# Kernel optimization log

Measured on AMD Instinct MI355X. Metric: run time of the kernel, lower is better.

Reference implementation:

```python
import jax, jax.numpy as jnp
import numpy as np

B, QT, N, E, H = 4, 1024, 2048, 512, 8
Dh = E // H
ROPE_BASE = 10000.0


def rope_cos_sin_from_pos(pos_idx, Dh, base=10000.0, dtype=jnp.float32):
    # pos_idx: [B, T] -> cos, sin: [B, T, Dh]
    half = Dh // 2
    freqs = 1.0 / base ** (jnp.arange(0, half, dtype=dtype) / half)
    ang = pos_idx.astype(dtype)[..., None] * freqs[None, None, :]
    cos = jnp.repeat(jnp.cos(ang), 2, axis=-1)
    sin = jnp.repeat(jnp.sin(ang), 2, axis=-1)
    return cos, sin


def rope_apply(x_hd, cos, sin):
    # x_hd: [B, H, T, Dh]; cos/sin: [B, 1, T, Dh] (only first Dh//2 used, as in source)
    D = x_hd.shape[-1]
    x2 = x_hd.reshape(*x_hd.shape[:-1], D // 2, 2)
    x1, xi = x2[..., 0], x2[..., 1]
    c = cos[..., :D // 2]
    s = sin[..., :D // 2]
    y1 = x1 * c - xi * s
    y2 = x1 * s + xi * c
    return jnp.stack([y1, y2], axis=-1).reshape(*x_hd.shape)


def setup_inputs() -> dict:
    key = jax.random.key(0)
    ks = jax.random.split(key, 16)
    scale_w = 1.0 / np.sqrt(E)
    inp = {
        "q": jax.random.normal(ks[0], (B, QT, E), jnp.float32),
        "kv": jax.random.normal(ks[1], (B, N, E), jnp.float32),
        "q_mask": jax.random.randint(ks[2], (B, QT), 0, 2) > 0,
        "kv_mask": jax.random.randint(ks[3], (B, N), 0, 2) > 0,
        "q_pos_idx": jnp.sort(jax.random.randint(ks[4], (B, QT), 0, 4096), axis=-1).astype(jnp.int32),
        "kv_pos_idx": jnp.sort(jax.random.randint(ks[5], (B, N), 0, 4096), axis=-1).astype(jnp.int32),
        "Wq": jax.random.normal(ks[6], (E, E), jnp.float32) * scale_w,
        "bq": jnp.zeros((E,), jnp.float32),
        "Wk": jax.random.normal(ks[7], (E, E), jnp.float32) * scale_w,
        "bk": jnp.zeros((E,), jnp.float32),
        "Wv": jax.random.normal(ks[8], (E, E), jnp.float32) * scale_w,
        "bv": jnp.zeros((E,), jnp.float32),
        "Wo": jax.random.normal(ks[9], (E, E), jnp.float32) * scale_w,
        "bo": jnp.zeros((E,), jnp.float32),
    }
    return inp


def reference(q, kv, q_mask, kv_mask, q_pos_idx, kv_pos_idx,
              Wq, bq, Wk, bk, Wv, bv, Wo, bo):
    scale = 1.0 / jnp.sqrt(jnp.array(Dh, dtype=q.dtype))
    # projections -> [B, H, T, Dh]
    qh = (q @ Wq + bq).reshape(B, QT, H, Dh).transpose(0, 2, 1, 3)
    kh = (kv @ Wk + bk).reshape(B, N, H, Dh).transpose(0, 2, 1, 3)
    vh = (kv @ Wv + bv).reshape(B, N, H, Dh).transpose(0, 2, 1, 3)
    # per-sample RoPE
    cos_q, sin_q = rope_cos_sin_from_pos(q_pos_idx, Dh, ROPE_BASE, qh.dtype)
    cos_k, sin_k = rope_cos_sin_from_pos(kv_pos_idx, Dh, ROPE_BASE, kh.dtype)
    qh = rope_apply(qh, cos_q[:, None], sin_q[:, None])
    kh = rope_apply(kh, cos_k[:, None], sin_k[:, None])
    # scores [B, H, Q, N]
    scores = jnp.einsum("bhqd,bhkd->bhqk", qh, kh) * scale
    kvm = kv_mask[:, None, None, :].astype(bool)
    scores = jnp.where(kvm, scores, jnp.full_like(scores, -1e9))
    attn = jax.nn.softmax(scores, axis=-1)
    # dropout_rate=0 / deterministic -> identity; post-softmax mask + renorm
    attn = attn * kvm
    attn = attn / (attn.sum(-1, keepdims=True) + 1e-9)
    ctx = jnp.einsum("bhqk,bhkd->bhqd", attn, vh)
    ctx = ctx.transpose(0, 2, 1, 3).reshape(B, QT, E)
    ctx = ctx @ Wo + bo
    ctx = ctx * q_mask.astype(ctx.dtype)[:, :, None]
    return ctx, attn
```

## Files before the change

kernel.cpp:

```cpp
#include <hip/hip_runtime.h>
#include <hip/hip_bf16.h>

#define B_  4
#define QT_ 1024
#define N_  2048
#define E_  512
#define H_  8
#define DH_ 64

typedef float  f32x4  __attribute__((ext_vector_type(4)));
typedef __bf16 bf16x8 __attribute__((ext_vector_type(8)));
typedef unsigned short u16;
typedef u16 u16x4 __attribute__((ext_vector_type(4)));

static __device__ __forceinline__ u16 f2bf(float f) {
    unsigned u = __builtin_bit_cast(unsigned, f);
    return (u16)((u + 0x7fffu + ((u >> 16) & 1u)) >> 16);
}

static __device__ __forceinline__ bf16x8 ldbf8(const u16* p) {
    uint4 v = *reinterpret_cast<const uint4*>(p);
    return __builtin_bit_cast(bf16x8, v);
}

#define MFMA16(a, b, c) __builtin_amdgcn_mfma_f32_16x16x32_bf16((a), (b), (c), 0, 0, 0)

static __device__ __forceinline__ void g2lds16(const u16* g, u16* l) {
    __builtin_amdgcn_global_load_lds((__attribute__((address_space(1))) void*)(void*)g,
                                     (__attribute__((address_space(3))) void*)l, 16, 0, 0);
}

__global__ __launch_bounds__(256) void cvt_all(const float* __restrict__ q,
                                               const float* __restrict__ kv,
                                               u16* __restrict__ qbf,
                                               u16* __restrict__ kvbf) {
    const int QN4 = B_ * QT_ * E_ / 4;
    int i = blockIdx.x * 256 + threadIdx.x;
    const float4* s;
    ushort4* d;
    if (i < QN4) {
        s = reinterpret_cast<const float4*>(q) + i;
        d = reinterpret_cast<ushort4*>(qbf) + i;
    } else {
        int j = i - QN4;
        s = reinterpret_cast<const float4*>(kv) + j;
        d = reinterpret_cast<ushort4*>(kvbf) + j;
    }
    float4 v = *s;
    ushort4 o;
    o.x = f2bf(v.x); o.y = f2bf(v.y); o.z = f2bf(v.z); o.w = f2bf(v.w);
    *d = o;
}

__global__ __launch_bounds__(256) void wt_all(const float* __restrict__ Wq,
                                              const float* __restrict__ Wk,
                                              const float* __restrict__ Wv,
                                              const float* __restrict__ Wo,
                                              u16* __restrict__ wt4) {
    __shared__ float t[64][65];
    const float* W = (blockIdx.z == 0) ? Wq : (blockIdx.z == 1) ? Wk : (blockIdx.z == 2) ? Wv : Wo;
    u16* dst = wt4 + (size_t)blockIdx.z * E_ * E_;
    int k0 = blockIdx.x * 64, n0 = blockIdx.y * 64;
    int tid = threadIdx.x;
#pragma unroll
    for (int i = 0; i < 16; i++) {
        int idx = tid + i * 256, r = idx >> 6, c = idx & 63;
        t[r][c] = W[(k0 + r) * E_ + n0 + c];
    }
    __syncthreads();
#pragma unroll
    for (int i = 0; i < 16; i++) {
        int idx = tid + i * 256, r = idx >> 6, c = idx & 63;
        dst[(n0 + r) * E_ + k0 + c] = f2bf(t[c][r]);
    }
}

__global__ __launch_bounds__(256) void rope_all(const int* __restrict__ qpos,
                                                const int* __restrict__ kvpos,
                                                float2* __restrict__ tq,
                                                float2* __restrict__ tk) {
    const int QROWS = B_ * QT_;
    int i = blockIdx.x * 256 + threadIdx.x;
    int k = i & 15, row = i >> 4;
    float fr = exp2f((float)k * -0.41524101186092028f);
    int p;
    float2* dst;
    if (row < QROWS) { p = qpos[row]; dst = tq + i; }
    else { p = kvpos[row - QROWS]; dst = tk + (i - QROWS * 16); }
    float sn, cs;
    sincosf((float)p * fr, &sn, &cs);
    *dst = make_float2(cs, sn);
}

__global__ __launch_bounds__(256) void proj_qkv(const u16* __restrict__ qbf,
                                                const u16* __restrict__ kvbf,
                                                const u16* __restrict__ wt4,
                                                const float* __restrict__ bq,
                                                const float* __restrict__ bk,
                                                const float* __restrict__ bv,
                                                u16* __restrict__ qhh,
                                                u16* __restrict__ khh,
                                                u16* __restrict__ vt,
                                                const float2* __restrict__ tq,
                                                const float2* __restrict__ tk) {
    __shared__ __align__(16) u16 la[2][128 * 32];
    __shared__ __align__(16) u16 lb[2][128 * 32];

    const int id = blockIdx.x;
    const int sw = (id & 7) * 80 + (id >> 3);
    const bool isQ = (sw < 128);
    int m0, n0;
    const u16 *X, *W;
    if (isQ) { m0 = (sw >> 2) * 128; n0 = (sw & 3) * 128; X = qbf; W = wt4; }
    else { const int s2 = sw - 128; m0 = (s2 >> 3) * 128; n0 = (s2 & 7) * 128; X = kvbf; W = wt4 + 512 * 512; }

    const int tid = threadIdx.x, w = tid >> 6, lane = tid & 63;
    const int lr = lane & 15, lg = lane >> 4;
    const int wml = (w >> 1) * 64, wnl = (w & 1) * 64;

    auto stage = [&](const u16* gsrc, u16* lbuf) {
#pragma unroll
        for (int i = 0; i < 2; i++) {
            const int r0 = w * 32 + i * 16;
            const int row = r0 + (lane >> 2);
            const u16* src = gsrc + row * E_ + (((lane & 3) ^ (row & 3)) * 8);
            g2lds16(src, lbuf + r0 * 32);
        }
    };

    f32x4 acc[4][4];
#pragma unroll
    for (int i = 0; i < 4; i++)
#pragma unroll
        for (int j = 0; j < 4; j++) acc[i][j] = f32x4{0.f, 0.f, 0.f, 0.f};

    stage(X + m0 * E_, la[0]);
    stage(W + n0 * E_, lb[0]);
    __syncthreads();
    int buf = 0;
    for (int kt = 0; kt < E_ / 32; kt++) {
        if (kt + 1 < E_ / 32) {
            stage(X + m0 * E_ + (kt + 1) * 32, la[buf ^ 1]);
            stage(W + n0 * E_ + (kt + 1) * 32, lb[buf ^ 1]);
        }
        bf16x8 a[4], bb[4];
#pragma unroll
        for (int mb = 0; mb < 4; mb++) {
            const int r = wml + mb * 16 + lr;
            a[mb] = ldbf8(la[buf] + r * 32 + ((lg ^ (r & 3)) * 8));
        }
#pragma unroll
        for (int nb = 0; nb < 4; nb++) {
            const int r = wnl + nb * 16 + lr;
            bb[nb] = ldbf8(lb[buf] + r * 32 + ((lg ^ (r & 3)) * 8));
        }
        __builtin_amdgcn_s_setprio(1);
#pragma unroll
        for (int mb = 0; mb < 4; mb++)
#pragma unroll
            for (int nb = 0; nb < 4; nb++)
                acc[mb][nb] = MFMA16(a[mb], bb[nb], acc[mb][nb]);
        __builtin_amdgcn_s_setprio(0);
        __syncthreads();
        buf ^= 1;
    }

    const bool isV = !isQ && (n0 >= 512);
#pragma unroll
    for (int mb = 0; mb < 4; mb++) {
#pragma unroll
        for (int nb = 0; nb < 4; nb++) {
            const int col = n0 + wnl + nb * 16 + lr;
            const float bs = isQ ? bq[col] : (isV ? bv[col - 512] : bk[col]);
#pragma unroll
            for (int r = 0; r < 4; r++) {
                const int row = m0 + wml + mb * 16 + lg * 4 + r;
                float v = acc[mb][nb][r] + bs;
                if (isV) {
                    const int cv = col - 512, d = cv & 63, h = cv >> 6;
                    const int b = row >> 11, n = row & 2047;
                    vt[(((b * H_ + h) * (N_ / 64) + (n >> 6)) * DH_ + d) * 64 + (n & 63)] = f2bf(v);
                } else {
                    const int d = col & 63, h = col >> 6;
                    float2 t = isQ ? tq[row * 16 + (d >> 2)] : tk[row * 16 + (d >> 2)];
                    float other = __shfl_xor(v, 1);
                    float y = (d & 1) ? (other * t.y + v * t.x) : (v * t.x - other * t.y);
                    if (isQ) {
                        y *= 0.125f;
                        const int b = row >> 10, tok = row & 1023;
                        qhh[((b * H_ + h) * QT_ + tok) * DH_ + d] = f2bf(y);
                    } else {
                        const int b = row >> 11, tok = row & 2047;
                        khh[((b * H_ + h) * N_ + tok) * DH_ + d] = f2bf(y);
                    }
                }
            }
        }
    }
}

__global__ __launch_bounds__(256) void attn_sums(const u16* __restrict__ qh,
                                                 const u16* __restrict__ kh,
                                                 const int* __restrict__ kv_mask,
                                                 float* __restrict__ sums4) {
    __shared__ __align__(16) u16 kbuf[2][64 * 64];

    const int id = blockIdx.x;
    const int sw = (id & 7) * 256 + (id >> 3);
    const int bh = sw >> 6, qt = (sw >> 2) & 15, ns = sw & 3;
    const int b = bh >> 3;
    const int tid = threadIdx.x, w = tid >> 6, lane = tid & 63;
    const int lr = lane & 15, lg = lane >> 4;
    const int q0 = qt * 64 + w * 16;

    const u16* qbase = qh + (bh * QT_ + q0) * DH_;
    const bf16x8 qf0 = ldbf8(qbase + lr * DH_ + lg * 8);
    const bf16x8 qf1 = ldbf8(qbase + lr * DH_ + 32 + lg * 8);
    const u16* kbase = kh + (size_t)bh * (N_ * DH_) + ns * 512 * DH_;
    const int* mbase = kv_mask + b * N_ + ns * 512;

    auto stage = [&](const u16* gsrc, u16* lbuf) {
#pragma unroll
        for (int i = 0; i < 2; i++) {
            const int r0 = w * 16 + i * 8;
            const int row = r0 + (lane >> 3);
            const u16* src = gsrc + row * 64 + (((lane & 7) ^ (row & 7)) * 8);
            g2lds16(src, lbuf + r0 * 64);
        }
    };

    float lsum[4] = {0.f, 0.f, 0.f, 0.f};
    stage(kbase, kbuf[0]);
    __syncthreads();
    for (int t = 0; t < 8; t++) {
        const u16* kc = kbuf[t & 1];
        if (t < 7) stage(kbase + (t + 1) * (64 * DH_), kbuf[(t + 1) & 1]);
#pragma unroll
        for (int n = 0; n < 4; n++) {
            const int krow = n * 16 + lr;
            const u16* kp = kc + krow * 64;
            bf16x8 k0 = ldbf8(kp + ((lg ^ (krow & 7)) * 8));
            bf16x8 k1 = ldbf8(kp + (((lg + 4) ^ (krow & 7)) * 8));
            f32x4 c = f32x4{0.f, 0.f, 0.f, 0.f};
            __builtin_amdgcn_s_setprio(1);
            c = MFMA16(qf0, k0, c);
            c = MFMA16(qf1, k1, c);
            __builtin_amdgcn_s_setprio(0);
            const bool keep = (mbase[t * 64 + n * 16 + lr] != 0);
#pragma unroll
            for (int r = 0; r < 4; r++) lsum[r] += keep ? __expf(c[r]) : 0.f;
        }
        __syncthreads();
    }
#pragma unroll
    for (int r = 0; r < 4; r++) {
        float s = lsum[r];
        s += __shfl_xor(s, 1); s += __shfl_xor(s, 2);
        s += __shfl_xor(s, 4); s += __shfl_xor(s, 8);
        if (lr == 0) sums4[((size_t)bh * QT_ + q0 + lg * 4 + r) * 4 + ns] = s;
    }
}

__global__ __launch_bounds__(512) void attn_pv(const u16* __restrict__ qh,
                                               const u16* __restrict__ kh,
                                               const u16* __restrict__ vt,
                                               const int* __restrict__ kv_mask,
                                               const float* __restrict__ sums4,
                                               float* __restrict__ attn_out,
                                               float* __restrict__ pvpart) {
    __shared__ __align__(16) u16 kbuf[2][64 * 64];
    __shared__ __align__(16) u16 vbuf[2][64 * 64];
    __shared__ unsigned PW[8][16][32];

    const int id = blockIdx.x;
    const int sw = (id & 7) * 128 + (id >> 3);
    const int bh = sw >> 5, qt = (sw >> 2) & 7, ns = sw & 3;
    const int b = bh >> 3;
    const int tid = threadIdx.x, w = tid >> 6, lane = tid & 63;
    const int lr = lane & 15, lg = lane >> 4;
    const int q0 = qt * 128 + w * 16;

    const u16* qbase = qh + (bh * QT_ + q0) * DH_;
    const bf16x8 qf0 = ldbf8(qbase + lr * DH_ + lg * 8);
    const bf16x8 qf1 = ldbf8(qbase + lr * DH_ + 32 + lg * 8);
    const u16* kbase = kh + (size_t)bh * (N_ * DH_) + ns * 512 * DH_;
    const u16* vbase = vt + (size_t)bh * (N_ * DH_) + ns * 512 * DH_;
    const int* mbase = kv_mask + b * N_ + ns * 512;

    float inv[4];
#pragma unroll
    for (int r = 0; r < 4; r++) {
        float4 s4 = *reinterpret_cast<const float4*>(
            sums4 + ((size_t)bh * QT_ + q0 + lg * 4 + r) * 4);
        float tot = s4.x + s4.y + s4.z + s4.w;
        inv[r] = (tot > 0.f) ? (1.0f / tot) : 0.f;
    }

    auto stage = [&](int t, u16* kb, u16* vb) {
        const int r0 = w * 8;
        const int row = r0 + (lane >> 3);
        const int gsw = ((lane & 7) ^ (row & 7)) * 8;
        g2lds16(kbase + (t * 64 + row) * 64 + gsw, kb + r0 * 64);
        g2lds16(vbase + (t * 64 + row) * 64 + gsw, vb + r0 * 64);
    };

    f32x4 pv[4];
#pragma unroll
    for (int i = 0; i < 4; i++) pv[i] = f32x4{0.f, 0.f, 0.f, 0.f};
    unsigned(*P)[32] = PW[w];
    float* abase = attn_out + ((size_t)(bh * QT_ + q0)) * N_ + ns * 512;
    const int srow = lane >> 4, cq = lane & 15;

    stage(0, kbuf[0], vbuf[0]);
    __syncthreads();
    for (int t = 0; t < 8; t++) {
        const u16* kc = kbuf[t & 1];
        const u16* vc = vbuf[t & 1];
        if (t < 7) stage(t + 1, kbuf[(t + 1) & 1], vbuf[(t + 1) & 1]);
#pragma unroll
        for (int n = 0; n < 4; n++) {
            const int krow = n * 16 + lr;
            const u16* kp = kc + krow * 64;
            bf16x8 k0 = ldbf8(kp + ((lg ^ (krow & 7)) * 8));
            bf16x8 k1 = ldbf8(kp + (((lg + 4) ^ (krow & 7)) * 8));
            f32x4 c = f32x4{0.f, 0.f, 0.f, 0.f};
            __builtin_amdgcn_s_setprio(1);
            c = MFMA16(qf0, k0, c);
            c = MFMA16(qf1, k1, c);
            __builtin_amdgcn_s_setprio(0);
            const bool keep = (mbase[t * 64 + n * 16 + lr] != 0);
#pragma unroll
            for (int r = 0; r < 4; r++) {
                float p = keep ? (__expf(c[r]) * inv[r]) : 0.f;
                float hi = __shfl_xor(p, 1);
                __bf16 lo_b = (__bf16)p, hi_b = (__bf16)hi;
                unsigned pk = ((unsigned)__builtin_bit_cast(u16, hi_b) << 16) |
                              (unsigned)__builtin_bit_cast(u16, lo_b);
                if (!(lr & 1)) {
                    const int row = lg * 4 + r, c32 = n * 8 + (lr >> 1);
                    P[row][(((c32 >> 2) ^ (row & 7)) << 2) + (c32 & 3)] = pk;
                }
            }
        }
#pragma unroll
        for (int i = 0; i < 4; i++) {
            const int row = i * 4 + srow, rw = row & 7;
            const int m = (((cq >> 1) ^ rw) << 2) + ((cq & 1) << 1);
            uint2 pp = *reinterpret_cast<const uint2*>(&P[row][m]);
            f32x4 vv;
            vv[0] = __builtin_bit_cast(float, pp.x << 16);
            vv[1] = __builtin_bit_cast(float, pp.x & 0xffff0000u);
            vv[2] = __builtin_bit_cast(float, pp.y << 16);
            vv[3] = __builtin_bit_cast(float, pp.y & 0xffff0000u);
            *reinterpret_cast<f32x4*>(abase + (size_t)row * N_ + t * 64 + cq * 4) = vv;
        }
#pragma unroll
        for (int ks = 0; ks < 2; ks++) {
            const int g = (4 * ks + lg) ^ (lr & 7);
            uint4 a4 = *reinterpret_cast<const uint4*>(&P[lr][g << 2]);
            bf16x8 af = __builtin_bit_cast(bf16x8, a4);
            __builtin_amdgcn_s_setprio(1);
#pragma unroll
            for (int nb = 0; nb < 4; nb++) {
                const int vrow = nb * 16 + lr;
                bf16x8 bv = ldbf8(vc + vrow * 64 + (((ks * 4 + lg) ^ (vrow & 7)) * 8));
                pv[nb] = MFMA16(af, bv, pv[nb]);
            }
            __builtin_amdgcn_s_setprio(0);
        }
        __syncthreads();
    }

    float* pbase = pvpart + (((size_t)ns * 32 + bh) * QT_) * DH_;
#pragma unroll
    for (int nb = 0; nb < 4; nb++)
#pragma unroll
        for (int r = 0; r < 4; r++)
            pbase[(size_t)(q0 + lg * 4 + r) * DH_ + nb * 16 + lr] = pv[nb][r];
}

__global__ __launch_bounds__(256) void ctx_reduce(const float* __restrict__ pvpart,
                                                  u16* __restrict__ ctx) {
    const size_t SL = (size_t)32 * QT_ * DH_;
    const int i = blockIdx.x * 256 + threadIdx.x;
    const int base = i * 4;
    const int d = base & 63, h = (base >> 6) & 7;
    const int bt = base >> 9;
    const size_t pi = (((size_t)(bt >> 10) * 8 + h) * QT_ + (bt & 1023)) * DH_ + d;
    f32x4 s0 = *reinterpret_cast<const f32x4*>(pvpart + pi);
    f32x4 s1 = *reinterpret_cast<const f32x4*>(pvpart + SL + pi);
    f32x4 s2 = *reinterpret_cast<const f32x4*>(pvpart + 2 * SL + pi);
    f32x4 s3 = *reinterpret_cast<const f32x4*>(pvpart + 3 * SL + pi);
    u16x4 o;
#pragma unroll
    for (int j = 0; j < 4; j++) o[j] = f2bf((s0[j] + s1[j]) + (s2[j] + s3[j]));
    *reinterpret_cast<u16x4*>(ctx + base) = o;
}

__global__ __launch_bounds__(256) void proj_o(const u16* __restrict__ X,
                                              const u16* __restrict__ Wt,
                                              const float* __restrict__ bias,
                                              float* __restrict__ outp,
                                              const int* __restrict__ qmask) {
    __shared__ __align__(16) u16 la[2][64 * 64];
    __shared__ __align__(16) u16 lb[2][64 * 64];

    const int id = blockIdx.x;
    const int sw = (id & 7) * 64 + (id >> 3);
    const int m0 = (sw >> 3) * 64, n0 = (sw & 7) * 64;

    const int tid = threadIdx.x, w = tid >> 6, lane = tid & 63;
    const int lr = lane & 15, lg = lane >> 4;
    const int wml = (w >> 1) * 32, wnl = (w & 1) * 32;

    auto stage = [&](const u16* gsrc, u16* lbuf) {
#pragma unroll
        for (int i = 0; i < 2; i++) {
            const int r0 = w * 16 + i * 8;
            const int row = r0 + (lane >> 3);
            const u16* src = gsrc + row * E_ + (((lane & 7) ^ (row & 7)) * 8);
            g2lds16(src, lbuf + r0 * 64);
        }
    };

    f32x4 acc[2][2];
#pragma unroll
    for (int i = 0; i < 2; i++)
#pragma unroll
        for (int j = 0; j < 2; j++) acc[i][j] = f32x4{0.f, 0.f, 0.f, 0.f};

    stage(X + m0 * E_, la[0]);
    stage(Wt + n0 * E_, lb[0]);
    __syncthreads();
    int buf = 0;
    for (int kt = 0; kt < E_ / 64; kt++) {
        if (kt + 1 < E_ / 64) {
            stage(X + m0 * E_ + (kt + 1) * 64, la[buf ^ 1]);
            stage(Wt + n0 * E_ + (kt + 1) * 64, lb[buf ^ 1]);
        }
#pragma unroll
        for (int ks = 0; ks < 2; ks++) {
            bf16x8 a[2], bb[2];
#pragma unroll
            for (int mb = 0; mb < 2; mb++) {
                const int r = wml + mb * 16 + lr;
                a[mb] = ldbf8(la[buf] + r * 64 + (((ks * 4 + lg) ^ (r & 7)) * 8));
            }
#pragma unroll
            for (int nb = 0; nb < 2; nb++) {
                const int r = wnl + nb * 16 + lr;
                bb[nb] = ldbf8(lb[buf] + r * 64 + (((ks * 4 + lg) ^ (r & 7)) * 8));
            }
            __builtin_amdgcn_s_setprio(1);
#pragma unroll
            for (int mb = 0; mb < 2; mb++)
#pragma unroll
                for (int nb = 0; nb < 2; nb++)
                    acc[mb][nb] = MFMA16(a[mb], bb[nb], acc[mb][nb]);
            __builtin_amdgcn_s_setprio(0);
        }
        __syncthreads();
        buf ^= 1;
    }

#pragma unroll
    for (int mb = 0; mb < 2; mb++) {
#pragma unroll
        for (int nb = 0; nb < 2; nb++) {
            const int col = n0 + wnl + nb * 16 + lr;
            const float bs = bias[col];
#pragma unroll
            for (int r = 0; r < 4; r++) {
                const int row = m0 + wml + mb * 16 + lg * 4 + r;
                float v = acc[mb][nb][r] + bs;
                float m = (qmask[row] != 0) ? 1.0f : 0.0f;
                outp[row * E_ + col] = v * m;
            }
        }
    }
}

extern "C" void kernel_launch(void* const* d_in, const int* in_sizes, int n_in,
                              void* d_out, int out_size, void* d_ws, size_t ws_size,
                              hipStream_t stream) {
    (void)in_sizes; (void)n_in; (void)out_size; (void)ws_size;
    const float* q   = (const float*)d_in[0];
    const float* kv  = (const float*)d_in[1];
    const int* q_mask  = (const int*)d_in[2];
    const int* kv_mask = (const int*)d_in[3];
    const int* q_pos   = (const int*)d_in[4];
    const int* kv_pos  = (const int*)d_in[5];
    const float* Wq = (const float*)d_in[6];  const float* bq = (const float*)d_in[7];
    const float* Wk = (const float*)d_in[8];  const float* bk = (const float*)d_in[9];
    const float* Wv = (const float*)d_in[10]; const float* bv = (const float*)d_in[11];
    const float* Wo = (const float*)d_in[12]; const float* bo = (const float*)d_in[13];
    float* outp = (float*)d_out;

    char* ws = (char*)d_ws;
    size_t off = 0;
    auto carve = [&](size_t bytes) -> void* {
        void* p = ws + off;
        off = (off + bytes + 255) & ~(size_t)255;
        return p;
    };
    u16* qbf    = (u16*)carve((size_t)B_ * QT_ * E_ * 2);
    u16* kvbf   = (u16*)carve((size_t)B_ * N_ * E_ * 2);
    u16* wt4    = (u16*)carve((size_t)4 * E_ * E_ * 2);
    u16* qhh    = (u16*)carve((size_t)B_ * H_ * QT_ * DH_ * 2);
    u16* khh    = (u16*)carve((size_t)B_ * H_ * N_ * DH_ * 2);
    u16* vt     = (u16*)carve((size_t)B_ * H_ * DH_ * N_ * 2);
    u16* ctx    = (u16*)carve((size_t)B_ * QT_ * E_ * 2);
    float2* tq  = (float2*)carve((size_t)B_ * QT_ * 16 * sizeof(float2));
    float2* tk  = (float2*)carve((size_t)B_ * N_ * 16 * sizeof(float2));
    float* sums4  = (float*)carve((size_t)B_ * H_ * QT_ * 4 * sizeof(float));
    float* pvpart = (float*)carve((size_t)4 * B_ * H_ * QT_ * DH_ * sizeof(float));

    cvt_all<<<6144, 256, 0, stream>>>(q, kv, qbf, kvbf);
    wt_all<<<dim3(8, 8, 4), 256, 0, stream>>>(Wq, Wk, Wv, Wo, wt4);
    rope_all<<<768, 256, 0, stream>>>(q_pos, kv_pos, tq, tk);

    proj_qkv<<<640, 256, 0, stream>>>(qbf, kvbf, wt4, bq, bk, bv, qhh, khh, vt, tq, tk);

    attn_sums<<<2048, 256, 0, stream>>>(qhh, khh, kv_mask, sums4);
    attn_pv<<<1024, 512, 0, stream>>>(qhh, khh, vt, kv_mask, sums4,
                                      outp + (size_t)B_ * QT_ * E_, pvpart);
    ctx_reduce<<<2048, 256, 0, stream>>>(pvpart, ctx);

    proj_o<<<512, 256, 0, stream>>>(ctx, wt4 + 3 * 512 * 512, bo, outp, q_mask);
}
```

Before: 159.0 us.

## Double query rows per warp in attn_pv and fuse prep kernels

Each warp in attn_pv now handles 32 query rows instead of 16. Every K and V fragment read from LDS feeds two MFMAs, halving K/V staging traffic per query, and the grid shrinks to 512 blocks. The three preprocessing kernels (convert to bf16, weight transpose, RoPE table) are merged into one launch to cut launch overhead. The trade-off is higher register pressure, a larger P scratch buffer in LDS, and fewer blocks to fill the GPU.

```diff
diff --git a/kernel.cpp b/kernel.cpp
--- a/kernel.cpp
+++ b/kernel.cpp
@@ -30,66 +30,68 @@
                                      (__attribute__((address_space(3))) void*)l, 16, 0, 0);
 }
 
-__global__ __launch_bounds__(256) void cvt_all(const float* __restrict__ q,
-                                               const float* __restrict__ kv,
-                                               u16* __restrict__ qbf,
-                                               u16* __restrict__ kvbf) {
-    const int QN4 = B_ * QT_ * E_ / 4;
-    int i = blockIdx.x * 256 + threadIdx.x;
-    const float4* s;
-    ushort4* d;
-    if (i < QN4) {
-        s = reinterpret_cast<const float4*>(q) + i;
-        d = reinterpret_cast<ushort4*>(qbf) + i;
-    } else {
-        int j = i - QN4;
-        s = reinterpret_cast<const float4*>(kv) + j;
-        d = reinterpret_cast<ushort4*>(kvbf) + j;
-    }
-    float4 v = *s;
-    ushort4 o;
-    o.x = f2bf(v.x); o.y = f2bf(v.y); o.z = f2bf(v.z); o.w = f2bf(v.w);
-    *d = o;
-}
-
-__global__ __launch_bounds__(256) void wt_all(const float* __restrict__ Wq,
-                                              const float* __restrict__ Wk,
-                                              const float* __restrict__ Wv,
-                                              const float* __restrict__ Wo,
-                                              u16* __restrict__ wt4) {
-    __shared__ float t[64][65];
-    const float* W = (blockIdx.z == 0) ? Wq : (blockIdx.z == 1) ? Wk : (blockIdx.z == 2) ? Wv : Wo;
-    u16* dst = wt4 + (size_t)blockIdx.z * E_ * E_;
-    int k0 = blockIdx.x * 64, n0 = blockIdx.y * 64;
-    int tid = threadIdx.x;
-#pragma unroll
-    for (int i = 0; i < 16; i++) {
-        int idx = tid + i * 256, r = idx >> 6, c = idx & 63;
-        t[r][c] = W[(k0 + r) * E_ + n0 + c];
-    }
-    __syncthreads();
-#pragma unroll
-    for (int i = 0; i < 16; i++) {
-        int idx = tid + i * 256, r = idx >> 6, c = idx & 63;
-        dst[(n0 + r) * E_ + k0 + c] = f2bf(t[c][r]);
-    }
-}
-
-__global__ __launch_bounds__(256) void rope_all(const int* __restrict__ qpos,
+__global__ __launch_bounds__(256) void prep_all(const float* __restrict__ q,
+                                                const float* __restrict__ kv,
+                                                const float* __restrict__ Wq,
+                                                const float* __restrict__ Wk,
+                                                const float* __restrict__ Wv,
+                                                const float* __restrict__ Wo,
+                                                const int* __restrict__ qpos,
                                                 const int* __restrict__ kvpos,
+                                                u16* __restrict__ qbf,
+                                                u16* __restrict__ kvbf,
+                                                u16* __restrict__ wt4,
                                                 float2* __restrict__ tq,
                                                 float2* __restrict__ tk) {
-    const int QROWS = B_ * QT_;
-    int i = blockIdx.x * 256 + threadIdx.x;
-    int k = i & 15, row = i >> 4;
-    float fr = exp2f((float)k * -0.41524101186092028f);
-    int p;
-    float2* dst;
-    if (row < QROWS) { p = qpos[row]; dst = tq + i; }
-    else { p = kvpos[row - QROWS]; dst = tk + (i - QROWS * 16); }
-    float sn, cs;
-    sincosf((float)p * fr, &sn, &cs);
-    *dst = make_float2(cs, sn);
+    __shared__ float t[64][65];
+    const int bid = blockIdx.x, tid = threadIdx.x;
+    if (bid < 6144) {
+        const int QN4 = B_ * QT_ * E_ / 4;
+        int i = bid * 256 + tid;
+        const float4* s;
+        ushort4* d;
+        if (i < QN4) {
+            s = reinterpret_cast<const float4*>(q) + i;
+            d = reinterpret_cast<ushort4*>(qbf) + i;
+        } else {
+            int j = i - QN4;
+            s = reinterpret_cast<const float4*>(kv) + j;
+            d = reinterpret_cast<ushort4*>(kvbf) + j;
+        }
+        float4 v = *s;
+        ushort4 o;
+        o.x = f2bf(v.x); o.y = f2bf(v.y); o.z = f2bf(v.z); o.w = f2bf(v.w);
+        *d = o;
+    } else if (bid < 6400) {
+        const int idx = bid - 6144;
+        const int z = idx >> 6, rem = idx & 63, xb = rem & 7, yb = rem >> 3;
+        const float* W = (z == 0) ? Wq : (z == 1) ? Wk : (z == 2) ? Wv : Wo;
+        u16* dst = wt4 + (size_t)z * E_ * E_;
+        const int k0 = xb * 64, n0 = yb * 64;
+#pragma unroll
+        for (int i = 0; i < 16; i++) {
+            int ix = tid + i * 256, r = ix >> 6, c = ix & 63;
+            t[r][c] = W[(k0 + r) * E_ + n0 + c];
+        }
+        __syncthreads();
+#pragma unroll
+        for (int i = 0; i < 16; i++) {
+            int ix = tid + i * 256, r = ix >> 6, c = ix & 63;
+            dst[(n0 + r) * E_ + k0 + c] = f2bf(t[c][r]);
+        }
+    } else {
+        const int QROWS = B_ * QT_;
+        int i = (bid - 6400) * 256 + tid;
+        int k = i & 15, row = i >> 4;
+        float fr = exp2f((float)k * -0.41524101186092028f);
+        int p;
+        float2* dst;
+        if (row < QROWS) { p = qpos[row]; dst = tq + i; }
+        else { p = kvpos[row - QROWS]; dst = tk + (i - QROWS * 16); }
+        float sn, cs;
+        sincosf((float)p * fr, &sn, &cs);
+        *dst = make_float2(cs, sn);
+    }
 }
 
 __global__ __launch_bounds__(256) void proj_qkv(const u16* __restrict__ qbf,
@@ -261,40 +263,46 @@
     }
 }
 
-__global__ __launch_bounds__(512) void attn_pv(const u16* __restrict__ qh,
-                                               const u16* __restrict__ kh,
-                                               const u16* __restrict__ vt,
-                                               const int* __restrict__ kv_mask,
-                                               const float* __restrict__ sums4,
-                                               float* __restrict__ attn_out,
-                                               float* __restrict__ pvpart) {
+__global__ __launch_bounds__(512, 4) void attn_pv(const u16* __restrict__ qh,
+                                                  const u16* __restrict__ kh,
+                                                  const u16* __restrict__ vt,
+                                                  const int* __restrict__ kv_mask,
+                                                  const float* __restrict__ sums4,
+                                                  float* __restrict__ attn_out,
+                                                  float* __restrict__ pvpart) {
     __shared__ __align__(16) u16 kbuf[2][64 * 64];
     __shared__ __align__(16) u16 vbuf[2][64 * 64];
-    __shared__ unsigned PW[8][16][32];
+    __shared__ unsigned PW[8][32][32];
 
     const int id = blockIdx.x;
-    const int sw = (id & 7) * 128 + (id >> 3);
-    const int bh = sw >> 5, qt = (sw >> 2) & 7, ns = sw & 3;
+    const int sw = (id & 7) * 64 + (id >> 3);
+    const int bh = sw >> 4, qt = (sw >> 2) & 3, ns = sw & 3;
     const int b = bh >> 3;
     const int tid = threadIdx.x, w = tid >> 6, lane = tid & 63;
     const int lr = lane & 15, lg = lane >> 4;
-    const int q0 = qt * 128 + w * 16;
+    const int q0 = qt * 256 + w * 32;
 
     const u16* qbase = qh + (bh * QT_ + q0) * DH_;
-    const bf16x8 qf0 = ldbf8(qbase + lr * DH_ + lg * 8);
-    const bf16x8 qf1 = ldbf8(qbase + lr * DH_ + 32 + lg * 8);
+    bf16x8 qf[2][2];
+#pragma unroll
+    for (int mq = 0; mq < 2; mq++) {
+        qf[mq][0] = ldbf8(qbase + (mq * 16 + lr) * DH_ + lg * 8);
+        qf[mq][1] = ldbf8(qbase + (mq * 16 + lr) * DH_ + 32 + lg * 8);
+    }
     const u16* kbase = kh + (size_t)bh * (N_ * DH_) + ns * 512 * DH_;
     const u16* vbase = vt + (size_t)bh * (N_ * DH_) + ns * 512 * DH_;
     const int* mbase = kv_mask + b * N_ + ns * 512;
 
-    float inv[4];
-#pragma unroll
-    for (int r = 0; r < 4; r++) {
-        float4 s4 = *reinterpret_cast<const float4*>(
-            sums4 + ((size_t)bh * QT_ + q0 + lg * 4 + r) * 4);
-        float tot = s4.x + s4.y + s4.z + s4.w;
-        inv[r] = (tot > 0.f) ? (1.0f / tot) : 0.f;
-    }
+    float inv[2][4];
+#pragma unroll
+    for (int mq = 0; mq < 2; mq++)
+#pragma unroll
+        for (int r = 0; r < 4; r++) {
+            float4 s4 = *reinterpret_cast<const float4*>(
+                sums4 + ((size_t)bh * QT_ + q0 + mq * 16 + lg * 4 + r) * 4);
+            float tot = s4.x + s4.y + s4.z + s4.w;
+            inv[mq][r] = (tot > 0.f) ? (1.0f / tot) : 0.f;
+        }
 
     auto stage = [&](int t, u16* kb, u16* vb) {
         const int r0 = w * 8;
@@ -304,9 +312,11 @@
         g2lds16(vbase + (t * 64 + row) * 64 + gsw, vb + r0 * 64);
     };
 
-    f32x4 pv[4];
-#pragma unroll
-    for (int i = 0; i < 4; i++) pv[i] = f32x4{0.f, 0.f, 0.f, 0.f};
+    f32x4 pv[2][4];
+#pragma unroll
+    for (int mq = 0; mq < 2; mq++)
+#pragma unroll
+        for (int i = 0; i < 4; i++) pv[mq][i] = f32x4{0.f, 0.f, 0.f, 0.f};
     unsigned(*P)[32] = PW[w];
     float* abase = attn_out + ((size_t)(bh * QT_ + q0)) * N_ + ns * 512;
     const int srow = lane >> 4, cq = lane & 15;
@@ -323,27 +333,33 @@
             const u16* kp = kc + krow * 64;
             bf16x8 k0 = ldbf8(kp + ((lg ^ (krow & 7)) * 8));
             bf16x8 k1 = ldbf8(kp + (((lg + 4) ^ (krow & 7)) * 8));
-            f32x4 c = f32x4{0.f, 0.f, 0.f, 0.f};
+            f32x4 c0 = f32x4{0.f, 0.f, 0.f, 0.f};
+            f32x4 c1 = f32x4{0.f, 0.f, 0.f, 0.f};
             __builtin_amdgcn_s_setprio(1);
-            c = MFMA16(qf0, k0, c);
-            c = MFMA16(qf1, k1, c);
+            c0 = MFMA16(qf[0][0], k0, c0);
+            c0 = MFMA16(qf[0][1], k1, c0);
+            c1 = MFMA16(qf[1][0], k0, c1);
+            c1 = MFMA16(qf[1][1], k1, c1);
             __builtin_amdgcn_s_setprio(0);
-            const bool keep = (mbase[t * 64 + n * 16 + lr] != 0);
-#pragma unroll
-            for (int r = 0; r < 4; r++) {
-                float p = keep ? (__expf(c[r]) * inv[r]) : 0.f;
-                float hi = __shfl_xor(p, 1);
-                __bf16 lo_b = (__bf16)p, hi_b = (__bf16)hi;
-                unsigned pk = ((unsigned)__builtin_bit_cast(u16, hi_b) << 16) |
-                              (unsigned)__builtin_bit_cast(u16, lo_b);
-                if (!(lr & 1)) {
-                    const int row = lg * 4 + r, c32 = n * 8 + (lr >> 1);
-                    P[row][(((c32 >> 2) ^ (row & 7)) << 2) + (c32 & 3)] = pk;
+            const bool keep = (mbase[t * 64 + krow] != 0);
+#pragma unroll
+            for (int mq = 0; mq < 2; mq++) {
+#pragma unroll
+                for (int r = 0; r < 4; r++) {
+                    float p = keep ? (__expf((mq ? c1 : c0)[r]) * inv[mq][r]) : 0.f;
+                    float hi = __shfl_xor(p, 1);
+                    __bf16 lo_b = (__bf16)p, hi_b = (__bf16)hi;
+                    unsigned pk = ((unsigned)__builtin_bit_cast(u16, hi_b) << 16) |
+                                  (unsigned)__builtin_bit_cast(u16, lo_b);
+                    if (!(lr & 1)) {
+                        const int row = mq * 16 + lg * 4 + r, c32 = n * 8 + (lr >> 1);
+                        P[row][(((c32 >> 2) ^ (row & 7)) << 2) + (c32 & 3)] = pk;
+                    }
                 }
             }
         }
 #pragma unroll
-        for (int i = 0; i < 4; i++) {
+        for (int i = 0; i < 8; i++) {
             const int row = i * 4 + srow, rw = row & 7;
             const int m = (((cq >> 1) ^ rw) << 2) + ((cq & 1) << 1);
             uint2 pp = *reinterpret_cast<const uint2*>(&P[row][m]);
@@ -356,27 +372,35 @@
         }
 #pragma unroll
         for (int ks = 0; ks < 2; ks++) {
-            const int g = (4 * ks + lg) ^ (lr & 7);
-            uint4 a4 = *reinterpret_cast<const uint4*>(&P[lr][g << 2]);
-            bf16x8 af = __builtin_bit_cast(bf16x8, a4);
-            __builtin_amdgcn_s_setprio(1);
+            bf16x8 bv[4];
 #pragma unroll
             for (int nb = 0; nb < 4; nb++) {
                 const int vrow = nb * 16 + lr;
-                bf16x8 bv = ldbf8(vc + vrow * 64 + (((ks * 4 + lg) ^ (vrow & 7)) * 8));
-                pv[nb] = MFMA16(af, bv, pv[nb]);
-            }
-            __builtin_amdgcn_s_setprio(0);
+                bv[nb] = ldbf8(vc + vrow * 64 + (((ks * 4 + lg) ^ (vrow & 7)) * 8));
+            }
+            const int g = (4 * ks + lg) ^ (lr & 7);
+#pragma unroll
+            for (int mq = 0; mq < 2; mq++) {
+                uint4 a4 = *reinterpret_cast<const uint4*>(&P[mq * 16 + lr][g << 2]);
+                bf16x8 af = __builtin_bit_cast(bf16x8, a4);
+                __builtin_amdgcn_s_setprio(1);
+#pragma unroll
+                for (int nb = 0; nb < 4; nb++)
+                    pv[mq][nb] = MFMA16(af, bv[nb], pv[mq][nb]);
+                __builtin_amdgcn_s_setprio(0);
+            }
         }
         __syncthreads();
     }
 
     float* pbase = pvpart + (((size_t)ns * 32 + bh) * QT_) * DH_;
 #pragma unroll
-    for (int nb = 0; nb < 4; nb++)
-#pragma unroll
-        for (int r = 0; r < 4; r++)
-            pbase[(size_t)(q0 + lg * 4 + r) * DH_ + nb * 16 + lr] = pv[nb][r];
+    for (int mq = 0; mq < 2; mq++)
+#pragma unroll
+        for (int nb = 0; nb < 4; nb++)
+#pragma unroll
+            for (int r = 0; r < 4; r++)
+                pbase[(size_t)(q0 + mq * 16 + lg * 4 + r) * DH_ + nb * 16 + lr] = pv[mq][nb][r];
 }
 
 __global__ __launch_bounds__(256) void ctx_reduce(const float* __restrict__ pvpart,
@@ -515,15 +539,14 @@
     float* sums4  = (float*)carve((size_t)B_ * H_ * QT_ * 4 * sizeof(float));
     float* pvpart = (float*)carve((size_t)4 * B_ * H_ * QT_ * DH_ * sizeof(float));
 
-    cvt_all<<<6144, 256, 0, stream>>>(q, kv, qbf, kvbf);
-    wt_all<<<dim3(8, 8, 4), 256, 0, stream>>>(Wq, Wk, Wv, Wo, wt4);
-    rope_all<<<768, 256, 0, stream>>>(q_pos, kv_pos, tq, tk);
+    prep_all<<<7168, 256, 0, stream>>>(q, kv, Wq, Wk, Wv, Wo, q_pos, kv_pos,
+                                       qbf, kvbf, wt4, tq, tk);
 
     proj_qkv<<<640, 256, 0, stream>>>(qbf, kvbf, wt4, bq, bk, bv, qhh, khh, vt, tq, tk);
 
     attn_sums<<<2048, 256, 0, stream>>>(qhh, khh, kv_mask, sums4);
-    attn_pv<<<1024, 512, 0, stream>>>(qhh, khh, vt, kv_mask, sums4,
-                                      outp + (size_t)B_ * QT_ * E_, pvpart);
+    attn_pv<<<512, 512, 0, stream>>>(qhh, khh, vt, kv_mask, sums4,
+                                     outp + (size_t)B_ * QT_ * E_, pvpart);
     ctx_reduce<<<2048, 256, 0, stream>>>(pvpart, ctx);
 
     proj_o<<<512, 256, 0, stream>>>(ctx, wt4 + 3 * 512 * 512, bo, outp, q_mask);
```

Result: faster. 153.5 us (-3.4%).
